# Performance work log

Hardware: AMD Instinct MI355X
Metric: run time of the kernel (lower is better)

## Reference

```python
import jax, jax.numpy as jnp
import numpy as np

B, J, M, D = 32, 256, 128, 200
P = 3  # processing_steps


def setup_inputs() -> dict:
    key = jax.random.key(0)
    ks = jax.random.split(key, 8)
    def w(k, shape, fan_in):
        return jax.random.normal(k, shape, jnp.float32) / np.sqrt(fan_in).astype(np.float32)
    return {
        "cos": jax.random.normal(ks[0], (B, J, M), jnp.float32),      # speaker_cos_index[i][j] rows
        "bank_s": jax.random.normal(ks[1], (J, B, D), jnp.float32),   # bank_s[j][i]
        "mem_a": jax.random.normal(ks[2], (B, M, D), jnp.float32),    # speaker A memory
        "mem_b": jax.random.normal(ks[3], (B, M, D), jnp.float32),    # speaker B memory
        "w_fc": w(ks[4], (D, D), D),
        "b_fc": jnp.zeros((D,), jnp.float32),
        "w_fc1": w(ks[5], (D, 2 * D), 2 * D),
        "b_fc1": jnp.zeros((D,), jnp.float32),
        "w_ih": w(ks[6], (4 * D, D), D),   # torch LSTM gate order: i, f, g, o
        "w_hh": w(ks[7], (4 * D, D), D),
        "b_ih": jnp.zeros((4 * D,), jnp.float32),
        "b_hh": jnp.zeros((4 * D,), jnp.float32),
    }


def _forward(cos, bank_s, mem_a, mem_b, w_fc, b_fc, w_fc1, b_fc1, w_ih, w_hh, b_ih, b_hh):
    Jn = bank_s.shape[0]
    flags = jnp.arange(Jn) % 2       # alternating speakers A,B,A,B,...
    slots = jnp.arange(Jn) // 2      # per-speaker running slot counter (A_count/B_count)

    def fc(x):
        return x @ w_fc.T + b_fc

    def step(carry, xs):
        ma, mb = carry                     # [B, M, D] each
        cos_j, bank_j, flag, slot = xs     # [B,M], [B,D], scalar, scalar
        mem = jnp.where(flag == 0, ma, mb)
        # a = cos_row @ memory -> LSTM initial hidden state
        h = jnp.einsum('bm,bmd->bd', cos_j, mem)
        c = jnp.zeros_like(h)
        q = fc(bank_j)                     # q_t = fc(bank_s[j][i])
        for _ in range(P):
            gates = q @ w_ih.T + b_ih + h @ w_hh.T + b_hh   # [B, 4D]
            i_g, f_g, g_g, o_g = jnp.split(gates, 4, axis=-1)
            c = jax.nn.sigmoid(f_g) * c + jax.nn.sigmoid(i_g) * jnp.tanh(g_g)
            h = jax.nn.sigmoid(o_g) * jnp.tanh(c)
            att = jax.nn.softmax(jnp.einsum('bd,bmd->bm', h, mem), axis=-1)
            x = jnp.einsum('bm,bmd->bd', att, mem)
            q = jnp.concatenate([x, q], axis=-1) @ w_fc1.T + b_fc1
        # gated scatter-update of the current speaker's memory slot
        slot_vec = mem[:, slot]            # [B, D]
        z = jnp.tanh(fc(q) + fc(slot_vec))
        mem_new = mem.at[:, slot].set(z * slot_vec)
        ma = jnp.where(flag == 0, mem_new, ma)
        mb = jnp.where(flag == 0, mb, mem_new)
        return (ma, mb), q

    xs = (jnp.swapaxes(cos, 0, 1), bank_s, flags, slots)
    _, outs = jax.lax.scan(step, (mem_a, mem_b), xs)   # outs: [J, B, D]
    return jnp.swapaxes(outs, 0, 1)                    # [B, J, D] (length == J, no padding)


def reference(cos, bank_s, mem_a, mem_b, w_fc, b_fc, w_fc1, b_fc1, w_ih, w_hh, b_ih, b_hh):
    return _forward(cos, bank_s, mem_a, mem_b, w_fc, b_fc, w_fc1, b_fc1,
                    w_ih, w_hh, b_ih, b_hh)
```

## Files before the change

### kernel.cpp

```cpp
#include <hip/hip_runtime.h>
#include <stdint.h>

#define DD 200
#define MM 128
#define JJ 256
#define BB 32
#define TPB 1024
#define MEMSTRIDE 201

__device__ inline float sigm(float x) { return 1.f / (1.f + expf(-x)); }


__global__ void pack_gates_w(const float* __restrict__ w_ih, const float* __restrict__ w_hh,
                             const float* __restrict__ b_ih, const float* __restrict__ b_hh,
                             float4* __restrict__ Wg4, float* __restrict__ bg) {
  int idx = blockIdx.x * blockDim.x + threadIdx.x;
  if (idx < 100 * 800) {
    int k4 = idx / 800, g = idx - k4 * 800;
    float v[4];
    #pragma unroll
    for (int e = 0; e < 4; ++e) {
      int k = 4 * k4 + e;
      v[e] = (k < DD) ? w_ih[g * DD + k] : w_hh[g * DD + (k - DD)];
    }
    Wg4[idx] = make_float4(v[0], v[1], v[2], v[3]);
  }
  if (idx < 800) bg[idx] = b_ih[idx] + b_hh[idx];
}

__global__ void pack_fc1(const float* __restrict__ w_fc1, float4* __restrict__ Tfc14) {
  int idx = blockIdx.x * blockDim.x + threadIdx.x;
  if (idx < 100 * DD) {
    int k4 = idx / DD, d = idx - k4 * DD;
    const float* p = w_fc1 + d * 400 + 4 * k4;
    Tfc14[idx] = make_float4(p[0], p[1], p[2], p[3]);
  }
}

__global__ void pack_fc(const float* __restrict__ w_fc, float4* __restrict__ Tfc4) {
  int idx = blockIdx.x * blockDim.x + threadIdx.x;
  if (idx < 50 * DD) {
    int k4 = idx / DD, d = idx - k4 * DD;
    const float* p = w_fc + d * DD + 4 * k4;
    Tfc4[idx] = make_float4(p[0], p[1], p[2], p[3]);
  }
}

__global__ __launch_bounds__(TPB, 4)
void chain_kernel(const float* __restrict__ cosb, const float* __restrict__ bank,
                  const float* __restrict__ mem_a, const float* __restrict__ mem_b,
                  const float* __restrict__ b_fc, const float* __restrict__ b_fc1,
                  const float4* __restrict__ Wg4, const float4* __restrict__ Tfc14,
                  const float4* __restrict__ Tfc4, const float* __restrict__ bg,
                  float* __restrict__ out)
{
  extern __shared__ float mem_s[];
  __shared__ __align__(16) float qh_s[400];
  __shared__ __align__(16) float xq_s[400];
  __shared__ __align__(16) float qsv_s[DD];
  __shared__ __align__(16) float bank_sh[2][DD];
  __shared__ __align__(16) float q0_s[2][DD];
  __shared__ __align__(16) float cos_s[2][MM];
  __shared__ __align__(16) float gates_s[800];
  __shared__ __align__(16) float logp_s[1024];
  __shared__ __align__(16) float hp_s[400];
  __shared__ __align__(16) float xp_s[400];
  __shared__ __align__(16) float fq_s[400];
  __shared__ __align__(16) float att_s[MM];

  const int t = threadIdx.x;
  const int par = blockIdx.x & 1;
  const int b = blockIdx.x >> 1;

  const float* msrc = (par ? mem_b : mem_a) + b * MM * DD;
  for (int i = t; i < MM * DD; i += TPB) {
    int m = i / DD, d = i - m * DD;
    mem_s[m * MEMSTRIDE + d] = msrc[i];
  }
  if (t < MM) cos_s[0][t] = cosb[(b * JJ + par) * MM + t];
  else if (t < MM + DD) bank_sh[0][t - MM] = bank[(par * BB + b) * DD + (t - MM)];
  __syncthreads();

  if (t < DD) {
    float a0 = b_fc[t], a1 = 0.f, a2 = 0.f, a3 = 0.f;
    const float4* bv = reinterpret_cast<const float4*>(bank_sh[0]);
    const float4* wp = Tfc4 + t;
    #pragma unroll 5
    for (int k4 = 0; k4 < 50; ++k4) {
      float4 w = wp[k4 * DD], v = bv[k4];
      a0 = fmaf(w.x, v.x, a0); a1 = fmaf(w.y, v.y, a1);
      a2 = fmaf(w.z, v.z, a2); a3 = fmaf(w.w, v.w, a3);
    }
    q0_s[0][t] = (a0 + a1) + (a2 + a3);
  }
  __syncthreads();

  float c_reg = 0.f, sv_reg = 0.f;

  for (int s = 0; s < JJ / 2; ++s) {
    const int j = 2 * s + par;
    const int cur = s & 1, nxt = cur ^ 1;

    if (t < 400) {
      int half = (t >= DD) ? 1 : 0;
      int d = t - half * DD;
      const float* cs = cos_s[cur] + half * 64;
      const float* mp = mem_s + (half * 64) * MEMSTRIDE + d;
      float a0 = 0.f, a1 = 0.f;
      #pragma unroll 4
      for (int m = 0; m < 64; m += 2) {
        a0 = fmaf(cs[m], mp[m * MEMSTRIDE], a0);
        a1 = fmaf(cs[m + 1], mp[(m + 1) * MEMSTRIDE], a1);
      }
      hp_s[half * DD + d] = a0 + a1;
    } else if (t < 400 + MM + DD) {
      if (s + 1 < JJ / 2) {
        int u = t - 400, j2 = j + 2;
        if (u < MM) cos_s[nxt][u] = cosb[(b * JJ + j2) * MM + u];
        else bank_sh[nxt][u - MM] = bank[(j2 * BB + b) * DD + (u - MM)];
      }
    }
    __syncthreads();

    if (t < DD) {
      float h = hp_s[t] + hp_s[DD + t];
      float q = q0_s[cur][t];
      qh_s[200 + t] = h;
      qh_s[t] = q;
      xq_s[200 + t] = q;
      c_reg = 0.f;
    }
    __syncthreads();

    for (int p = 0; p < 3; ++p) {
      if (t < 800) {
        const float4* qv4 = reinterpret_cast<const float4*>(qh_s);
        const float4* wp = Wg4 + t;
        float a0 = bg[t], a1 = 0.f, a2 = 0.f, a3 = 0.f;
        for (int k4 = 0; k4 < 100; k4 += 4) {
          float4 w0 = wp[k4 * 800], w1 = wp[(k4 + 1) * 800];
          float4 w2 = wp[(k4 + 2) * 800], w3 = wp[(k4 + 3) * 800];
          float4 v0 = qv4[k4], v1 = qv4[k4 + 1], v2 = qv4[k4 + 2], v3 = qv4[k4 + 3];
          a0 = fmaf(w0.x, v0.x, a0); a0 = fmaf(w0.y, v0.y, a0);
          a0 = fmaf(w0.z, v0.z, a0); a0 = fmaf(w0.w, v0.w, a0);
          a1 = fmaf(w1.x, v1.x, a1); a1 = fmaf(w1.y, v1.y, a1);
          a1 = fmaf(w1.z, v1.z, a1); a1 = fmaf(w1.w, v1.w, a1);
          a2 = fmaf(w2.x, v2.x, a2); a2 = fmaf(w2.y, v2.y, a2);
          a2 = fmaf(w2.z, v2.z, a2); a2 = fmaf(w2.w, v2.w, a2);
          a3 = fmaf(w3.x, v3.x, a3); a3 = fmaf(w3.y, v3.y, a3);
          a3 = fmaf(w3.z, v3.z, a3); a3 = fmaf(w3.w, v3.w, a3);
        }
        gates_s[t] = (a0 + a1) + (a2 + a3);
      } else if (p == 0 && t >= 832 && s + 1 < JJ / 2) {
        int u = t - 832;
        for (int d = u; d < DD; d += 192) {
          float a0 = b_fc[d], a1 = 0.f, a2 = 0.f, a3 = 0.f;
          const float4* bv = reinterpret_cast<const float4*>(bank_sh[nxt]);
          const float4* wp = Tfc4 + d;
          #pragma unroll 5
          for (int k4 = 0; k4 < 50; ++k4) {
            float4 w = wp[k4 * DD], v = bv[k4];
            a0 = fmaf(w.x, v.x, a0); a1 = fmaf(w.y, v.y, a1);
            a2 = fmaf(w.z, v.z, a2); a3 = fmaf(w.w, v.w, a3);
          }
          q0_s[nxt][d] = (a0 + a1) + (a2 + a3);
        }
      }
      __syncthreads();

      if (t < DD) {
        float ig = gates_s[t], fg = gates_s[200 + t], gg = gates_s[400 + t], og = gates_s[600 + t];
        c_reg = sigm(fg) * c_reg + sigm(ig) * tanhf(gg);
        float h = sigm(og) * tanhf(c_reg);
        qh_s[200 + t] = h;
        xq_s[200 + t] = qh_s[t];
      }
      __syncthreads();

      {
        int qd = t >> 7, m = t & 127;
        const float* hv = qh_s + 200 + qd * 25;
        const float* mrow = mem_s + m * MEMSTRIDE + qd * 25;
        float l0 = 0.f, l1 = 0.f;
        #pragma unroll
        for (int d = 0; d < 24; d += 2) {
          l0 = fmaf(hv[d], mrow[d], l0);
          l1 = fmaf(hv[d + 1], mrow[d + 1], l1);
        }
        l0 = fmaf(hv[24], mrow[24], l0);
        logp_s[qd * 128 + m] = l0 + l1;
      }
      __syncthreads();

      if (t < 64) {
        float l0 = 0.f, l1 = 0.f;
        #pragma unroll
        for (int qd = 0; qd < 8; ++qd) {
          l0 += logp_s[qd * 128 + t];
          l1 += logp_s[qd * 128 + t + 64];
        }
        float mx = fmaxf(l0, l1);
        #pragma unroll
        for (int o = 1; o < 64; o <<= 1) mx = fmaxf(mx, __shfl_xor(mx, o));
        float e0 = expf(l0 - mx), e1 = expf(l1 - mx);
        float ssum = e0 + e1;
        #pragma unroll
        for (int o = 1; o < 64; o <<= 1) ssum += __shfl_xor(ssum, o);
        float inv = 1.f / ssum;
        att_s[t] = e0 * inv;
        att_s[t + 64] = e1 * inv;
      }
      __syncthreads();

      if (t < 400) {
        int half = (t >= DD) ? 1 : 0;
        int d = t - half * DD;
        const float* as = att_s + half * 64;
        const float* mp = mem_s + (half * 64) * MEMSTRIDE + d;
        float a0 = 0.f, a1 = 0.f;
        #pragma unroll 4
        for (int m = 0; m < 64; m += 2) {
          a0 = fmaf(as[m], mp[m * MEMSTRIDE], a0);
          a1 = fmaf(as[m + 1], mp[(m + 1) * MEMSTRIDE], a1);
        }
        xp_s[half * DD + d] = a0 + a1;
      }
      __syncthreads();

      if (t < 400) {
        int kh = (t >= DD) ? 1 : 0;
        int d = t - kh * DD;
        const float4* wp = Tfc14 + d;
        float a0 = 0.f, a1 = 0.f, a2 = 0.f, a3 = 0.f;
        if (kh == 0) {
          const float4* x0 = reinterpret_cast<const float4*>(xp_s);
          const float4* x1 = reinterpret_cast<const float4*>(xp_s + DD);
          #pragma unroll 5
          for (int k4 = 0; k4 < 50; ++k4) {
            float4 w = wp[k4 * DD];
            float4 va = x0[k4], vb = x1[k4];
            a0 = fmaf(w.x, va.x + vb.x, a0); a1 = fmaf(w.y, va.y + vb.y, a1);
            a2 = fmaf(w.z, va.z + vb.z, a2); a3 = fmaf(w.w, va.w + vb.w, a3);
          }
        } else {
          const float4* qv = reinterpret_cast<const float4*>(xq_s);
          #pragma unroll 5
          for (int k4 = 50; k4 < 100; ++k4) {
            float4 w = wp[k4 * DD], v = qv[k4];
            a0 = fmaf(w.x, v.x, a0); a1 = fmaf(w.y, v.y, a1);
            a2 = fmaf(w.z, v.z, a2); a3 = fmaf(w.w, v.w, a3);
          }
        }
        fq_s[kh * DD + d] = (a0 + a1) + (a2 + a3);
      }
      __syncthreads();

      if (t < DD) {
        float qn = fq_s[t] + fq_s[DD + t] + b_fc1[t];
        qh_s[t] = qn;
        if (p == 2) {
          out[(b * JJ + j) * DD + t] = qn;
          sv_reg = mem_s[s * MEMSTRIDE + t];
          qsv_s[t] = qn + sv_reg;
        }
      }
      __syncthreads();
    }

    if (t < 400) {
      int kh = (t >= DD) ? 1 : 0;
      int d = t - kh * DD;
      const float4* wp = Tfc4 + d;
      const float4* qv = reinterpret_cast<const float4*>(qsv_s);
      float a0 = 0.f, a1 = 0.f, a2 = 0.f, a3 = 0.f;
      #pragma unroll 5
      for (int k4 = kh * 25; k4 < kh * 25 + 25; ++k4) {
        float4 w = wp[k4 * DD], v = qv[k4];
        a0 = fmaf(w.x, v.x, a0); a1 = fmaf(w.y, v.y, a1);
        a2 = fmaf(w.z, v.z, a2); a3 = fmaf(w.w, v.w, a3);
      }
      fq_s[kh * DD + d] = (a0 + a1) + (a2 + a3);
    }
    __syncthreads();

    if (t < DD) {
      float z = tanhf(fq_s[t] + fq_s[DD + t] + 2.f * b_fc[t]);
      mem_s[s * MEMSTRIDE + t] = z * sv_reg;
    }
    __syncthreads();
  }
}

extern "C" void kernel_launch(void* const* d_in, const int* in_sizes, int n_in,
                              void* d_out, int out_size, void* d_ws, size_t ws_size,
                              hipStream_t stream) {
  const float* cosb  = (const float*)d_in[0];
  const float* bank  = (const float*)d_in[1];
  const float* mem_a = (const float*)d_in[2];
  const float* mem_b = (const float*)d_in[3];
  const float* w_fc  = (const float*)d_in[4];
  const float* b_fc  = (const float*)d_in[5];
  const float* w_fc1 = (const float*)d_in[6];
  const float* b_fc1 = (const float*)d_in[7];
  const float* w_ih  = (const float*)d_in[8];
  const float* w_hh  = (const float*)d_in[9];
  const float* b_ih  = (const float*)d_in[10];
  const float* b_hh  = (const float*)d_in[11];

  char* ws = (char*)d_ws;
  float4* Wg4   = (float4*)(ws);
  float4* Tfc14 = (float4*)(ws + 1280000);
  float4* Tfc4  = (float4*)(ws + 1600000);
  float*  bg    = (float*) (ws + 1760000);

  pack_gates_w<<<(100 * 800 + 255) / 256, 256, 0, stream>>>(w_ih, w_hh, b_ih, b_hh, Wg4, bg);
  pack_fc1<<<(100 * DD + 255) / 256, 256, 0, stream>>>(w_fc1, Tfc14);
  pack_fc<<<(50 * DD + 255) / 256, 256, 0, stream>>>(w_fc, Tfc4);

  int dynbytes = MM * MEMSTRIDE * sizeof(float);
  hipFuncSetAttribute(reinterpret_cast<const void*>(chain_kernel),
                      hipFuncAttributeMaxDynamicSharedMemorySize, dynbytes);
  chain_kernel<<<64, TPB, dynbytes, stream>>>(cosb, bank, mem_a, mem_b, b_fc, b_fc1,
                                              Wg4, Tfc14, Tfc4, bg, (float*)d_out);
}
```

Measured before the change: 7.091 ms.

## Prefetch first weight chunks across barriers and use lightweight LDS-only barriers

```diff
diff --git a/kernel.cpp b/kernel.cpp
--- a/kernel.cpp
+++ b/kernel.cpp
@@ -8,41 +8,56 @@
 #define TPB 1024
 #define MEMSTRIDE 201
 
+#define SOFTBAR() asm volatile("s_waitcnt lgkmcnt(0)\n\ts_barrier" ::: "memory")
+
+typedef float f4 __attribute__((ext_vector_type(4)));
+
 __device__ inline float sigm(float x) { return 1.f / (1.f + expf(-x)); }
+
+__device__ inline void fma4spread(float& a0, float& a1, float& a2, float& a3, f4 w, f4 v) {
+  a0 = fmaf(w[0], v[0], a0); a1 = fmaf(w[1], v[1], a1);
+  a2 = fmaf(w[2], v[2], a2); a3 = fmaf(w[3], v[3], a3);
+}
+
+__device__ inline float dot4acc(float acc, f4 w, f4 v) {
+  acc = fmaf(w[0], v[0], acc); acc = fmaf(w[1], v[1], acc);
+  acc = fmaf(w[2], v[2], acc); acc = fmaf(w[3], v[3], acc);
+  return acc;
+}
 
 
 __global__ void pack_gates_w(const float* __restrict__ w_ih, const float* __restrict__ w_hh,
                              const float* __restrict__ b_ih, const float* __restrict__ b_hh,
-                             float4* __restrict__ Wg4, float* __restrict__ bg) {
+                             float* __restrict__ Wg4, float* __restrict__ bg) {
   int idx = blockIdx.x * blockDim.x + threadIdx.x;
   if (idx < 100 * 800) {
     int k4 = idx / 800, g = idx - k4 * 800;
-    float v[4];
     #pragma unroll
     for (int e = 0; e < 4; ++e) {
       int k = 4 * k4 + e;
-      v[e] = (k < DD) ? w_ih[g * DD + k] : w_hh[g * DD + (k - DD)];
-    }
-    Wg4[idx] = make_float4(v[0], v[1], v[2], v[3]);
+      Wg4[4 * idx + e] = (k < DD) ? w_ih[g * DD + k] : w_hh[g * DD + (k - DD)];
+    }
   }
   if (idx < 800) bg[idx] = b_ih[idx] + b_hh[idx];
 }
 
-__global__ void pack_fc1(const float* __restrict__ w_fc1, float4* __restrict__ Tfc14) {
+__global__ void pack_fc1(const float* __restrict__ w_fc1, float* __restrict__ Tfc14) {
   int idx = blockIdx.x * blockDim.x + threadIdx.x;
   if (idx < 100 * DD) {
     int k4 = idx / DD, d = idx - k4 * DD;
     const float* p = w_fc1 + d * 400 + 4 * k4;
-    Tfc14[idx] = make_float4(p[0], p[1], p[2], p[3]);
-  }
-}
-
-__global__ void pack_fc(const float* __restrict__ w_fc, float4* __restrict__ Tfc4) {
+    #pragma unroll
+    for (int e = 0; e < 4; ++e) Tfc14[4 * idx + e] = p[e];
+  }
+}
+
+__global__ void pack_fc(const float* __restrict__ w_fc, float* __restrict__ Tfc4) {
   int idx = blockIdx.x * blockDim.x + threadIdx.x;
   if (idx < 50 * DD) {
     int k4 = idx / DD, d = idx - k4 * DD;
     const float* p = w_fc + d * DD + 4 * k4;
-    Tfc4[idx] = make_float4(p[0], p[1], p[2], p[3]);
+    #pragma unroll
+    for (int e = 0; e < 4; ++e) Tfc4[4 * idx + e] = p[e];
   }
 }
 
@@ -50,8 +65,8 @@
 void chain_kernel(const float* __restrict__ cosb, const float* __restrict__ bank,
                   const float* __restrict__ mem_a, const float* __restrict__ mem_b,
                   const float* __restrict__ b_fc, const float* __restrict__ b_fc1,
-                  const float4* __restrict__ Wg4, const float4* __restrict__ Tfc14,
-                  const float4* __restrict__ Tfc4, const float* __restrict__ bg,
+                  const f4* __restrict__ Wg4, const f4* __restrict__ Tfc14,
+                  const f4* __restrict__ Tfc4, const float* __restrict__ bg,
                   float* __restrict__ out)
 {
   extern __shared__ float mem_s[];
@@ -72,6 +87,12 @@
   const int par = blockIdx.x & 1;
   const int b = blockIdx.x >> 1;
 
+  const f4* wpC = Wg4 + t;
+  const int khH = (t >= DD) ? 1 : 0;
+  const int dH = t - khH * DD;
+  const f4* wpH2 = Tfc14 + dH + khH * 50 * DD;
+  const f4* wpK2 = Tfc4 + dH + khH * 25 * DD;
+
   const float* msrc = (par ? mem_b : mem_a) + b * MM * DD;
   for (int i = t; i < MM * DD; i += TPB) {
     int m = i / DD, d = i - m * DD;
@@ -83,13 +104,11 @@
 
   if (t < DD) {
     float a0 = b_fc[t], a1 = 0.f, a2 = 0.f, a3 = 0.f;
-    const float4* bv = reinterpret_cast<const float4*>(bank_sh[0]);
-    const float4* wp = Tfc4 + t;
+    const f4* bv = reinterpret_cast<const f4*>(bank_sh[0]);
+    const f4* wp = Tfc4 + t;
     #pragma unroll 5
     for (int k4 = 0; k4 < 50; ++k4) {
-      float4 w = wp[k4 * DD], v = bv[k4];
-      a0 = fmaf(w.x, v.x, a0); a1 = fmaf(w.y, v.y, a1);
-      a2 = fmaf(w.z, v.z, a2); a3 = fmaf(w.w, v.w, a3);
+      fma4spread(a0, a1, a2, a3, wp[k4 * DD], bv[k4]);
     }
     q0_s[0][t] = (a0 + a1) + (a2 + a3);
   }
@@ -100,6 +119,9 @@
   for (int s = 0; s < JJ / 2; ++s) {
     const int j = 2 * s + par;
     const int cur = s & 1, nxt = cur ^ 1;
+    f4 cp0 = {0,0,0,0}, cp1 = {0,0,0,0}, cp2 = {0,0,0,0}, cp3 = {0,0,0,0};
+    f4 cp4 = {0,0,0,0}, cp5 = {0,0,0,0}, cp6 = {0,0,0,0}, cp7 = {0,0,0,0};
+    f4 kp0 = {0,0,0,0}, kp1 = {0,0,0,0}, kp2 = {0,0,0,0}, kp3 = {0,0,0,0};
 
     if (t < 400) {
       int half = (t >= DD) ? 1 : 0;
@@ -120,7 +142,7 @@
         else bank_sh[nxt][u - MM] = bank[(j2 * BB + b) * DD + (u - MM)];
       }
     }
-    __syncthreads();
+    SOFTBAR();
 
     if (t < DD) {
       float h = hp_s[t] + hp_s[DD + t];
@@ -130,43 +152,47 @@
       xq_s[200 + t] = q;
       c_reg = 0.f;
     }
-    __syncthreads();
+    if (t < 800) {
+      cp0 = wpC[0];        cp1 = wpC[800];      cp2 = wpC[2 * 800]; cp3 = wpC[3 * 800];
+      cp4 = wpC[4 * 800];  cp5 = wpC[5 * 800];  cp6 = wpC[6 * 800]; cp7 = wpC[7 * 800];
+    }
+    SOFTBAR();
 
     for (int p = 0; p < 3; ++p) {
       if (t < 800) {
-        const float4* qv4 = reinterpret_cast<const float4*>(qh_s);
-        const float4* wp = Wg4 + t;
+        const f4* qv4 = reinterpret_cast<const f4*>(qh_s);
         float a0 = bg[t], a1 = 0.f, a2 = 0.f, a3 = 0.f;
-        for (int k4 = 0; k4 < 100; k4 += 4) {
-          float4 w0 = wp[k4 * 800], w1 = wp[(k4 + 1) * 800];
-          float4 w2 = wp[(k4 + 2) * 800], w3 = wp[(k4 + 3) * 800];
-          float4 v0 = qv4[k4], v1 = qv4[k4 + 1], v2 = qv4[k4 + 2], v3 = qv4[k4 + 3];
-          a0 = fmaf(w0.x, v0.x, a0); a0 = fmaf(w0.y, v0.y, a0);
-          a0 = fmaf(w0.z, v0.z, a0); a0 = fmaf(w0.w, v0.w, a0);
-          a1 = fmaf(w1.x, v1.x, a1); a1 = fmaf(w1.y, v1.y, a1);
-          a1 = fmaf(w1.z, v1.z, a1); a1 = fmaf(w1.w, v1.w, a1);
-          a2 = fmaf(w2.x, v2.x, a2); a2 = fmaf(w2.y, v2.y, a2);
-          a2 = fmaf(w2.z, v2.z, a2); a2 = fmaf(w2.w, v2.w, a2);
-          a3 = fmaf(w3.x, v3.x, a3); a3 = fmaf(w3.y, v3.y, a3);
-          a3 = fmaf(w3.z, v3.z, a3); a3 = fmaf(w3.w, v3.w, a3);
+        a0 = dot4acc(a0, cp0, qv4[0]);
+        a1 = dot4acc(a1, cp1, qv4[1]);
+        a2 = dot4acc(a2, cp2, qv4[2]);
+        a3 = dot4acc(a3, cp3, qv4[3]);
+        a0 = dot4acc(a0, cp4, qv4[4]);
+        a1 = dot4acc(a1, cp5, qv4[5]);
+        a2 = dot4acc(a2, cp6, qv4[6]);
+        a3 = dot4acc(a3, cp7, qv4[7]);
+        for (int k4 = 8; k4 < 100; k4 += 4) {
+          f4 w0 = wpC[k4 * 800], w1 = wpC[(k4 + 1) * 800];
+          f4 w2 = wpC[(k4 + 2) * 800], w3 = wpC[(k4 + 3) * 800];
+          a0 = dot4acc(a0, w0, qv4[k4]);
+          a1 = dot4acc(a1, w1, qv4[k4 + 1]);
+          a2 = dot4acc(a2, w2, qv4[k4 + 2]);
+          a3 = dot4acc(a3, w3, qv4[k4 + 3]);
         }
         gates_s[t] = (a0 + a1) + (a2 + a3);
       } else if (p == 0 && t >= 832 && s + 1 < JJ / 2) {
         int u = t - 832;
         for (int d = u; d < DD; d += 192) {
           float a0 = b_fc[d], a1 = 0.f, a2 = 0.f, a3 = 0.f;
-          const float4* bv = reinterpret_cast<const float4*>(bank_sh[nxt]);
-          const float4* wp = Tfc4 + d;
+          const f4* bv = reinterpret_cast<const f4*>(bank_sh[nxt]);
+          const f4* wp = Tfc4 + d;
           #pragma unroll 5
           for (int k4 = 0; k4 < 50; ++k4) {
-            float4 w = wp[k4 * DD], v = bv[k4];
-            a0 = fmaf(w.x, v.x, a0); a1 = fmaf(w.y, v.y, a1);
-            a2 = fmaf(w.z, v.z, a2); a3 = fmaf(w.w, v.w, a3);
+            fma4spread(a0, a1, a2, a3, wp[k4 * DD], bv[k4]);
           }
           q0_s[nxt][d] = (a0 + a1) + (a2 + a3);
         }
       }
-      __syncthreads();
+      SOFTBAR();
 
       if (t < DD) {
         float ig = gates_s[t], fg = gates_s[200 + t], gg = gates_s[400 + t], og = gates_s[600 + t];
@@ -175,8 +201,12 @@
         qh_s[200 + t] = h;
         xq_s[200 + t] = qh_s[t];
       }
-      __syncthreads();
-
+      SOFTBAR();
+
+      f4 hq0 = {0,0,0,0}, hq1 = {0,0,0,0}, hq2 = {0,0,0,0}, hq3 = {0,0,0,0};
+      if (t < 400) {
+        hq0 = wpH2[0]; hq1 = wpH2[DD]; hq2 = wpH2[2 * DD]; hq3 = wpH2[3 * DD];
+      }
       {
         int qd = t >> 7, m = t & 127;
         const float* hv = qh_s + 200 + qd * 25;
@@ -190,7 +220,7 @@
         l0 = fmaf(hv[24], mrow[24], l0);
         logp_s[qd * 128 + m] = l0 + l1;
       }
-      __syncthreads();
+      SOFTBAR();
 
       if (t < 64) {
         float l0 = 0.f, l1 = 0.f;
@@ -210,7 +240,7 @@
         att_s[t] = e0 * inv;
         att_s[t + 64] = e1 * inv;
       }
-      __syncthreads();
+      SOFTBAR();
 
       if (t < 400) {
         int half = (t >= DD) ? 1 : 0;
@@ -225,35 +255,35 @@
         }
         xp_s[half * DD + d] = a0 + a1;
       }
-      __syncthreads();
+      SOFTBAR();
 
       if (t < 400) {
-        int kh = (t >= DD) ? 1 : 0;
-        int d = t - kh * DD;
-        const float4* wp = Tfc14 + d;
         float a0 = 0.f, a1 = 0.f, a2 = 0.f, a3 = 0.f;
-        if (kh == 0) {
-          const float4* x0 = reinterpret_cast<const float4*>(xp_s);
-          const float4* x1 = reinterpret_cast<const float4*>(xp_s + DD);
-          #pragma unroll 5
-          for (int k4 = 0; k4 < 50; ++k4) {
-            float4 w = wp[k4 * DD];
-            float4 va = x0[k4], vb = x1[k4];
-            a0 = fmaf(w.x, va.x + vb.x, a0); a1 = fmaf(w.y, va.y + vb.y, a1);
-            a2 = fmaf(w.z, va.z + vb.z, a2); a3 = fmaf(w.w, va.w + vb.w, a3);
+        if (khH == 0) {
+          const f4* x0 = reinterpret_cast<const f4*>(xp_s);
+          const f4* x1 = reinterpret_cast<const f4*>(xp_s + DD);
+          fma4spread(a0, a1, a2, a3, hq0, x0[0] + x1[0]);
+          fma4spread(a0, a1, a2, a3, hq1, x0[1] + x1[1]);
+          fma4spread(a0, a1, a2, a3, hq2, x0[2] + x1[2]);
+          fma4spread(a0, a1, a2, a3, hq3, x0[3] + x1[3]);
+          #pragma unroll 2
+          for (int k4 = 4; k4 < 50; ++k4) {
+            fma4spread(a0, a1, a2, a3, wpH2[k4 * DD], x0[k4] + x1[k4]);
           }
         } else {
-          const float4* qv = reinterpret_cast<const float4*>(xq_s);
-          #pragma unroll 5
-          for (int k4 = 50; k4 < 100; ++k4) {
-            float4 w = wp[k4 * DD], v = qv[k4];
-            a0 = fmaf(w.x, v.x, a0); a1 = fmaf(w.y, v.y, a1);
-            a2 = fmaf(w.z, v.z, a2); a3 = fmaf(w.w, v.w, a3);
+          const f4* qv = reinterpret_cast<const f4*>(xq_s);
+          fma4spread(a0, a1, a2, a3, hq0, qv[50]);
+          fma4spread(a0, a1, a2, a3, hq1, qv[51]);
+          fma4spread(a0, a1, a2, a3, hq2, qv[52]);
+          fma4spread(a0, a1, a2, a3, hq3, qv[53]);
+          #pragma unroll 2
+          for (int kk = 4; kk < 50; ++kk) {
+            fma4spread(a0, a1, a2, a3, wpH2[kk * DD], qv[50 + kk]);
           }
         }
-        fq_s[kh * DD + d] = (a0 + a1) + (a2 + a3);
-      }
-      __syncthreads();
+        fq_s[khH * DD + dH] = (a0 + a1) + (a2 + a3);
+      }
+      SOFTBAR();
 
       if (t < DD) {
         float qn = fq_s[t] + fq_s[DD + t] + b_fc1[t];
@@ -264,30 +294,37 @@
           qsv_s[t] = qn + sv_reg;
         }
       }
-      __syncthreads();
+      if (p < 2) {
+        if (t < 800) {
+          cp0 = wpC[0];        cp1 = wpC[800];      cp2 = wpC[2 * 800]; cp3 = wpC[3 * 800];
+          cp4 = wpC[4 * 800];  cp5 = wpC[5 * 800];  cp6 = wpC[6 * 800]; cp7 = wpC[7 * 800];
+        }
+      } else if (t < 400) {
+        kp0 = wpK2[0]; kp1 = wpK2[DD]; kp2 = wpK2[2 * DD]; kp3 = wpK2[3 * DD];
+      }
+      SOFTBAR();
     }
 
     if (t < 400) {
-      int kh = (t >= DD) ? 1 : 0;
-      int d = t - kh * DD;
-      const float4* wp = Tfc4 + d;
-      const float4* qv = reinterpret_cast<const float4*>(qsv_s);
+      const f4* qv = reinterpret_cast<const f4*>(qsv_s);
       float a0 = 0.f, a1 = 0.f, a2 = 0.f, a3 = 0.f;
-      #pragma unroll 5
-      for (int k4 = kh * 25; k4 < kh * 25 + 25; ++k4) {
-        float4 w = wp[k4 * DD], v = qv[k4];
-        a0 = fmaf(w.x, v.x, a0); a1 = fmaf(w.y, v.y, a1);
-        a2 = fmaf(w.z, v.z, a2); a3 = fmaf(w.w, v.w, a3);
-      }
-      fq_s[kh * DD + d] = (a0 + a1) + (a2 + a3);
-    }
-    __syncthreads();
+      fma4spread(a0, a1, a2, a3, kp0, qv[khH * 25]);
+      fma4spread(a0, a1, a2, a3, kp1, qv[khH * 25 + 1]);
+      fma4spread(a0, a1, a2, a3, kp2, qv[khH * 25 + 2]);
+      fma4spread(a0, a1, a2, a3, kp3, qv[khH * 25 + 3]);
+      #pragma unroll 3
+      for (int kk = 4; kk < 25; ++kk) {
+        fma4spread(a0, a1, a2, a3, wpK2[kk * DD], qv[khH * 25 + kk]);
+      }
+      fq_s[khH * DD + dH] = (a0 + a1) + (a2 + a3);
+    }
+    SOFTBAR();
 
     if (t < DD) {
       float z = tanhf(fq_s[t] + fq_s[DD + t] + 2.f * b_fc[t]);
       mem_s[s * MEMSTRIDE + t] = z * sv_reg;
     }
-    __syncthreads();
+    SOFTBAR();
   }
 }
 
@@ -308,18 +345,19 @@
   const float* b_hh  = (const float*)d_in[11];
 
   char* ws = (char*)d_ws;
-  float4* Wg4   = (float4*)(ws);
-  float4* Tfc14 = (float4*)(ws + 1280000);
-  float4* Tfc4  = (float4*)(ws + 1600000);
-  float*  bg    = (float*) (ws + 1760000);
+  float* Wg4   = (float*)(ws);
+  float* Tfc14 = (float*)(ws + 1280000);
+  float* Tfc4  = (float*)(ws + 1600000);
+  float* bg    = (float*)(ws + 1760000);
 
   pack_gates_w<<<(100 * 800 + 255) / 256, 256, 0, stream>>>(w_ih, w_hh, b_ih, b_hh, Wg4, bg);
   pack_fc1<<<(100 * DD + 255) / 256, 256, 0, stream>>>(w_fc1, Tfc14);
   pack_fc<<<(50 * DD + 255) / 256, 256, 0, stream>>>(w_fc, Tfc4);
 
   int dynbytes = MM * MEMSTRIDE * sizeof(float);
-  hipFuncSetAttribute(reinterpret_cast<const void*>(chain_kernel),
-                      hipFuncAttributeMaxDynamicSharedMemorySize, dynbytes);
+  (void)hipFuncSetAttribute(reinterpret_cast<const void*>(chain_kernel),
+                            hipFuncAttributeMaxDynamicSharedMemorySize, dynbytes);
   chain_kernel<<<64, TPB, dynbytes, stream>>>(cosb, bank, mem_a, mem_b, b_fc, b_fc1,
-                                              Wg4, Tfc14, Tfc4, bg, (float*)d_out);
-}
+                                              (const f4*)Wg4, (const f4*)Tfc14,
+                                              (const f4*)Tfc4, bg, (float*)d_out);
+}
```

Result: slower. 10.89 ms (+53.6%).
